# Optimization experiments

Hardware: AMD Instinct MI355X
Metric: run time of the kernel (lower is better)

## Reference

```python
import jax, jax.numpy as jnp
import numpy as np

IN_CH = 512
SCALES = (128.0, 256.0, 512.0)
ASPECT_RATIOS = (0.5, 1.0, 2.0)
NUM_ANCHORS = 9
PRE_NMS_TOPK = 10000
POST_NMS_TOPK = 2000
NMS_THRESH = 0.7


def conv2d(x, w, b, pad):
    y = jax.lax.conv_general_dilated(
        x, w, window_strides=(1, 1), padding=[(pad, pad), (pad, pad)],
        dimension_numbers=('NCHW', 'OIHW', 'NCHW'))
    return y + b[None, :, None, None]


def generate_anchors(image_hw, feat_hw, dtype=jnp.float32):
    img_h, img_w = image_hw
    gh, gw = feat_hw
    stride_h = img_h // gh
    stride_w = img_w // gw
    scale = jnp.asarray(SCALES, dtype)
    ar = jnp.asarray(ASPECT_RATIOS, dtype)
    h_ratio = jnp.sqrt(ar)
    w_ratio = 1.0 / h_ratio
    ws = (w_ratio[:, None] * scale[None, :]).reshape(-1)  # (9,) ratio-major
    hs = (h_ratio[:, None] * scale[None, :]).reshape(-1)
    base = jnp.round(jnp.stack([-ws, -hs, ws, hs], axis=1) / 2.0)  # (9,4)
    shift_x = jnp.arange(gw, dtype=dtype) * stride_w
    shift_y = jnp.arange(gh, dtype=dtype) * stride_h
    sy, sx = jnp.meshgrid(shift_y, shift_x, indexing='ij')
    sx = sx.reshape(-1)
    sy = sy.reshape(-1)
    shifts = jnp.stack([sx, sy, sx, sy], axis=1)  # (gh*gw, 4)
    anchors = (shifts[:, None, :] + base[None, :, :]).reshape(-1, 4)
    return anchors


def decode_boxes(deltas, anchors):
    # deltas: (N,4) [dx,dy,dw,dh]; anchors: (N,4) [x1,y1,x2,y2]
    w = anchors[:, 2] - anchors[:, 0]
    h = anchors[:, 3] - anchors[:, 1]
    cx = anchors[:, 0] + 0.5 * w
    cy = anchors[:, 1] + 0.5 * h
    dx, dy, dw, dh = deltas[:, 0], deltas[:, 1], deltas[:, 2], deltas[:, 3]
    pcx = w * dx + cx
    pcy = h * dy + cy
    pw = jnp.exp(dw) * w
    ph = jnp.exp(dh) * h
    return jnp.stack([pcx - 0.5 * pw, pcy - 0.5 * ph,
                      pcx + 0.5 * pw, pcy + 0.5 * ph], axis=1)


def clamp_boxes(b, image_hw):
    h, w = image_hw
    return jnp.stack([jnp.clip(b[:, 0], 0.0, w), jnp.clip(b[:, 1], 0.0, h),
                      jnp.clip(b[:, 2], 0.0, w), jnp.clip(b[:, 3], 0.0, h)], axis=1)


def pairwise_iou(boxes1, boxes2):
    area1 = (boxes1[:, 2] - boxes1[:, 0]) * (boxes1[:, 3] - boxes1[:, 1])
    area2 = (boxes2[:, 2] - boxes2[:, 0]) * (boxes2[:, 3] - boxes2[:, 1])
    xl = jnp.maximum(boxes1[:, None, 0], boxes2[None, :, 0])
    yt = jnp.maximum(boxes1[:, None, 1], boxes2[None, :, 1])
    xr = jnp.minimum(boxes1[:, None, 2], boxes2[None, :, 2])
    yb = jnp.minimum(boxes1[:, None, 3], boxes2[None, :, 3])
    inter = jnp.clip(xr - xl, 0.0) * jnp.clip(yb - yt, 0.0)
    return inter / (area1[:, None] + area2[None, :] - inter)


def nms_keep(boxes_sorted, thresh):
    # boxes already sorted by score descending; returns bool keep mask
    n = boxes_sorted.shape[0]
    iou = pairwise_iou(boxes_sorted, boxes_sorted)  # (n,n) ~ the memory-bound hot spot
    idx = jnp.arange(n)
    def body(i, keep):
        suppressed = jnp.any((iou[i] > thresh) & keep & (idx < i))
        return keep.at[i].set(jnp.logical_not(suppressed))
    return jax.lax.fori_loop(0, n, body, jnp.ones((n,), dtype=bool))


def filter_proposals(proposals, logits, image_hw):
    scores = jax.nn.sigmoid(logits.reshape(-1))
    top_scores, top_idx = jax.lax.top_k(scores, PRE_NMS_TOPK)  # sorted descending
    props = proposals[top_idx]
    props = clamp_boxes(props, image_hw)
    keep = nms_keep(jax.lax.stop_gradient(props), NMS_THRESH)
    masked = jnp.where(keep, jax.lax.stop_gradient(top_scores), -1.0)
    sel_scores, sel = jax.lax.top_k(masked, POST_NMS_TOPK)
    valid = sel_scores >= 0.0  # sigmoid scores are >0; padded slots are -1
    out_boxes = jnp.where(valid[:, None], props[sel], 0.0)
    out_scores = jnp.where(valid, top_scores[sel], 0.0)
    return out_boxes, out_scores


def setup_inputs() -> dict:
    key = jax.random.key(0)
    ks = jax.random.split(key, 6)
    image = jax.random.normal(ks[0], (1, 3, 800, 800), jnp.float32)
    feat = jax.random.normal(ks[1], (1, IN_CH, 50, 50), jnp.float32)
    # small init scales keep exp(dw) numerically tame (mimics real conv init)
    rpn_w = jax.random.normal(ks[2], (IN_CH, IN_CH, 3, 3), jnp.float32) * 0.02
    rpn_b = jnp.zeros((IN_CH,), jnp.float32)
    cls_w = jax.random.normal(ks[3], (NUM_ANCHORS, IN_CH, 1, 1), jnp.float32) * 0.01
    cls_b = jnp.zeros((NUM_ANCHORS,), jnp.float32)
    box_w = jax.random.normal(ks[4], (NUM_ANCHORS * 4, IN_CH, 1, 1), jnp.float32) * 0.01
    box_b = jnp.zeros((NUM_ANCHORS * 4,), jnp.float32)
    return {"image": image, "feat": feat, "rpn_w": rpn_w, "rpn_b": rpn_b,
            "cls_w": cls_w, "cls_b": cls_b, "box_w": box_w, "box_b": box_b}


def reference(image, feat, rpn_w, rpn_b, cls_w, cls_b, box_w, box_b):
    B, _, H, W = feat.shape  # B == 1 as in the original (single-image RPN)
    rpn_feat = jax.nn.relu(conv2d(feat, rpn_w, rpn_b, pad=1))
    cls = conv2d(rpn_feat, cls_w, cls_b, pad=0)        # (1, 9, H, W)
    box = conv2d(rpn_feat, box_w, box_b, pad=0)        # (1, 36, H, W)
    anchors = generate_anchors(image.shape[-2:], (H, W), feat.dtype)  # (H*W*9, 4)
    # cls: NCHW -> NHWC -> (N_anchors, 1), anchor order = (y, x, anchor)
    cls_flat = jnp.transpose(cls, (0, 2, 3, 1)).reshape(-1, 1)
    # box: (1,9,4,H,W) -> (1,H,W,9,4) -> (N_anchors, 4)
    deltas = jnp.transpose(box.reshape(B, NUM_ANCHORS, 4, H, W), (0, 3, 4, 1, 2)).reshape(-1, 4)
    proposals = decode_boxes(deltas, anchors)
    props, scores = filter_proposals(proposals, jax.lax.stop_gradient(cls_flat), image.shape[-2:])
    return props, scores, cls_flat
```

## Files before the change

kernel.cpp:

```cpp
#include <hip/hip_runtime.h>
#include <cstdint>
#include <cstddef>


typedef unsigned long long ull;
typedef double d4 __attribute__((ext_vector_type(4)));

#define NANCH 9
#define NPIX  2500
#define CIN   512
#define COUT  512
#define KTOT  4608
#define KSEG  2304
#define NBOX  22500
#define TOPK1 10000
#define TOPK2 2000
#define WORDS 157
#define NHEAD 45
#define HPAD  48

__global__ __launch_bounds__(128, 3) void conv_gemm(const float* __restrict__ feat,
                                                    const float* __restrict__ w,
                                                    double* __restrict__ part) {
  const int p0  = blockIdx.x * 32;
  const int co0 = blockIdx.y * 64;
  const int z   = blockIdx.z;
  const int kseg0 = z * KSEG;
  __shared__ float As[2][32][40];
  __shared__ float Bs[2][32][72];
  const int tid  = threadIdx.x;
  const int lane = tid & 63;
  const int wave = tid >> 6;
  const int quad = lane >> 4;
  const int l16  = lane & 15;
  const int wp = wave * 16;
  const int plB = tid & 31;
  const int kB0 = tid >> 5;
  const int pB = p0 + plB;
  const int py = pB / 50, px = pB - py * 50;
  const int coA = tid >> 1;
  const int kA2 = (tid & 1) * 16;

  int pmap[4];
  {
    double av_p = (quad == 0) ? (double)(l16 + 1) : (quad == 1 ? 1.0 : 0.0);
    double bv_p = (quad == 0) ? 1.0 : (quad == 1 ? (double)(1000 * (l16 + 1)) : 0.0);
    d4 dp = (d4){0.0, 0.0, 0.0, 0.0};
    dp = __builtin_amdgcn_mfma_f64_16x16x4f64(av_p, bv_p, dp, 0, 0, 0);
#pragma unroll
    for (int r = 0; r < 4; ++r) {
      int iv = (int)(dp[r] + 0.5);
      int mm = iv % 1000 - 1;
      int nn = iv / 1000 - 1;
      pmap[r] = (mm & 255) | (nn << 8);
    }
  }

  d4 acc[4];
#pragma unroll
  for (int i = 0; i < 4; ++i) acc[i] = (d4){0.0, 0.0, 0.0, 0.0};

  const float* wbase = w + (size_t)(co0 + coA) * KTOT + kseg0 + kA2;
  const int NCH = KSEG / 32;

  {
    float4 w0[4];
#pragma unroll
    for (int q = 0; q < 4; ++q) w0[q] = *(const float4*)(wbase + 4 * q);
    float f0[8];
#pragma unroll
    for (int jj = 0; jj < 8; ++jj) {
      int k = kseg0 + kB0 + 4 * jj;
      int ci = k / 9, r = k - ci * 9, ky = r / 3, kx = r - ky * 3;
      int yy = py + ky - 1, xx = px + kx - 1;
      float v = 0.0f;
      if (pB < NPIX && yy >= 0 && yy < 50 && xx >= 0 && xx < 50)
        v = feat[ci * NPIX + yy * 50 + xx];
      f0[jj] = v;
    }
#pragma unroll
    for (int q = 0; q < 4; ++q) {
      Bs[0][kA2 + 4 * q + 0][coA] = w0[q].x;
      Bs[0][kA2 + 4 * q + 1][coA] = w0[q].y;
      Bs[0][kA2 + 4 * q + 2][coA] = w0[q].z;
      Bs[0][kA2 + 4 * q + 3][coA] = w0[q].w;
    }
#pragma unroll
    for (int jj = 0; jj < 8; ++jj) As[0][kB0 + 4 * jj][plB] = f0[jj];
  }
  float4 wb1[4];
#pragma unroll
  for (int q = 0; q < 4; ++q) wb1[q] = *(const float4*)(wbase + 32 + 4 * q);
  float fb1[8];
#pragma unroll
  for (int jj = 0; jj < 8; ++jj) {
    int k = kseg0 + 32 + kB0 + 4 * jj;
    int ci = k / 9, r = k - ci * 9, ky = r / 3, kx = r - ky * 3;
    int yy = py + ky - 1, xx = px + kx - 1;
    float v = 0.0f;
    if (pB < NPIX && yy >= 0 && yy < 50 && xx >= 0 && xx < 50)
      v = feat[ci * NPIX + yy * 50 + xx];
    fb1[jj] = v;
  }
  __syncthreads();

  for (int c = 0; c < NCH; ++c) {
    const int buf = c & 1;
    if (c + 1 < NCH) {
#pragma unroll
      for (int q = 0; q < 4; ++q) {
        Bs[buf ^ 1][kA2 + 4 * q + 0][coA] = wb1[q].x;
        Bs[buf ^ 1][kA2 + 4 * q + 1][coA] = wb1[q].y;
        Bs[buf ^ 1][kA2 + 4 * q + 2][coA] = wb1[q].z;
        Bs[buf ^ 1][kA2 + 4 * q + 3][coA] = wb1[q].w;
      }
#pragma unroll
      for (int jj = 0; jj < 8; ++jj)
        As[buf ^ 1][kB0 + 4 * jj][plB] = fb1[jj];
    }
    if (c + 2 < NCH) {
#pragma unroll
      for (int q = 0; q < 4; ++q)
        wb1[q] = *(const float4*)(wbase + (c + 2) * 32 + 4 * q);
#pragma unroll
      for (int jj = 0; jj < 8; ++jj) {
        int k = kseg0 + (c + 2) * 32 + kB0 + 4 * jj;
        int ci = k / 9, r = k - ci * 9, ky = r / 3, kx = r - ky * 3;
        int yy = py + ky - 1, xx = px + kx - 1;
        float v = 0.0f;
        if (pB < NPIX && yy >= 0 && yy < 50 && xx >= 0 && xx < 50)
          v = feat[ci * NPIX + yy * 50 + xx];
        fb1[jj] = v;
      }
    }
#pragma unroll
    for (int kk = 0; kk < 32; kk += 4) {
      double av  = (double)As[buf][kk + quad][wp + l16];
      double bv0 = (double)Bs[buf][kk + quad][ 0 + l16];
      double bv1 = (double)Bs[buf][kk + quad][16 + l16];
      double bv2 = (double)Bs[buf][kk + quad][32 + l16];
      double bv3 = (double)Bs[buf][kk + quad][48 + l16];
      acc[0] = __builtin_amdgcn_mfma_f64_16x16x4f64(av, bv0, acc[0], 0, 0, 0);
      acc[1] = __builtin_amdgcn_mfma_f64_16x16x4f64(av, bv1, acc[1], 0, 0, 0);
      acc[2] = __builtin_amdgcn_mfma_f64_16x16x4f64(av, bv2, acc[2], 0, 0, 0);
      acc[3] = __builtin_amdgcn_mfma_f64_16x16x4f64(av, bv3, acc[3], 0, 0, 0);
    }
    __syncthreads();
  }
  double* basez = part + (size_t)z * COUT * NPIX;
#pragma unroll
  for (int cj = 0; cj < 4; ++cj) {
#pragma unroll
    for (int r = 0; r < 4; ++r) {
      int mm = pmap[r] & 255, nn = pmap[r] >> 8;
      int p  = p0 + wp + mm;
      int co = co0 + cj * 16 + nn;
      if (p < NPIX) basez[(size_t)co * NPIX + p] = acc[cj][r];
    }
  }
}

__global__ __launch_bounds__(256) void heads_mm(
    const double* __restrict__ part, const float* __restrict__ rpn_b,
    const float* __restrict__ cls_w, const float* __restrict__ box_w,
    double* __restrict__ headsc) {
  const int lane = threadIdx.x & 63;
  const int o = __builtin_amdgcn_readfirstlane(blockIdx.y * 4 + (threadIdx.x >> 6));
  if (o >= NHEAD) return;
  const int p = blockIdx.x * 64 + lane;
  const bool act = p < NPIX;
  const int pp = act ? p : 0;
  const float* wsel = (o < 9) ? (cls_w + (size_t)o * CIN)
                              : (box_w + (size_t)(o - 9) * CIN);
  const double* p0 = part + pp;
  const double* p1 = part + (size_t)COUT * NPIX + pp;
  double acc = 0.0;
#pragma unroll 4
  for (int co = 0; co < CIN; ++co) {
    double v = p0[(size_t)co * NPIX] + p1[(size_t)co * NPIX] + (double)rpn_b[co];
    v = v > 0.0 ? v : 0.0;
    acc += (double)wsel[co] * v;
  }
  if (act) headsc[(size_t)p * HPAD + o] = acc;
}

__global__ __launch_bounds__(256) void decode_kernel(
    const double* __restrict__ headsc, const float* __restrict__ cls_b,
    const float* __restrict__ box_b, double* __restrict__ logits,
    double* __restrict__ boxesAll, float* __restrict__ out_cls) {
  int idx = blockIdx.x * blockDim.x + threadIdx.x;
  if (idx >= NBOX) return;
  int p = idx / 9, a = idx - p * 9;
  int y = p / 50, x = p - y * 50;
  double sx = 16.0 * (double)x, sy = 16.0 * (double)y;
  const double scs[3] = {128.0, 256.0, 512.0};
  const double ars[3] = {0.5, 1.0, 2.0};
  double ar = ars[a / 3], sc = scs[a - (a / 3) * 3];
  double hr = sqrt(ar), wr = 1.0 / hr;
  double wv = wr * sc, hv = hr * sc;
  double bx0 = rint(-wv * 0.5), by0 = rint(-hv * 0.5);
  double bx1 = rint(wv * 0.5), by1 = rint(hv * 0.5);
  double a0 = sx + bx0, a1 = sy + by0, a2 = sx + bx1, a3 = sy + by1;
  double wA = a2 - a0, hA = a3 - a1;
  double cx = a0 + 0.5 * wA, cy = a1 + 0.5 * hA;
  const double* hp = headsc + (size_t)p * HPAD;
  double dx = hp[9 + a * 4 + 0] + (double)box_b[a * 4 + 0];
  double dy = hp[9 + a * 4 + 1] + (double)box_b[a * 4 + 1];
  double dw = hp[9 + a * 4 + 2] + (double)box_b[a * 4 + 2];
  double dh = hp[9 + a * 4 + 3] + (double)box_b[a * 4 + 3];
  double pcx = wA * dx + cx, pcy = hA * dy + cy;
  double pw = exp(dw) * wA, ph = exp(dh) * hA;
  double b0 = pcx - 0.5 * pw, b1 = pcy - 0.5 * ph;
  double b2 = pcx + 0.5 * pw, b3 = pcy + 0.5 * ph;
  b0 = fmin(fmax(b0, 0.0), 800.0);
  b1 = fmin(fmax(b1, 0.0), 800.0);
  b2 = fmin(fmax(b2, 0.0), 800.0);
  b3 = fmin(fmax(b3, 0.0), 800.0);
  boxesAll[(size_t)idx * 4 + 0] = b0;
  boxesAll[(size_t)idx * 4 + 1] = b1;
  boxesAll[(size_t)idx * 4 + 2] = b2;
  boxesAll[(size_t)idx * 4 + 3] = b3;
  double L = hp[a] + (double)cls_b[a];
  logits[idx] = L;
  out_cls[idx] = (float)L;
}

__global__ __launch_bounds__(256) void rank_count(const double* __restrict__ logits,
                                                  int* __restrict__ ranks) {
  __shared__ double Ls[2048];
  int i = blockIdx.x * 256 + threadIdx.x;
  int j0 = blockIdx.y * 2048;
  int jn = NBOX - j0;
  if (jn > 2048) jn = 2048;
  for (int t = threadIdx.x; t < jn; t += 256) Ls[t] = logits[j0 + t];
  __syncthreads();
  if (i >= NBOX) return;
  double Li = logits[i];
  int cnt = 0;
  for (int t = 0; t < jn; ++t) {
    double Lj = Ls[t];
    int j = j0 + t;
    cnt += (Lj > Li || (Lj == Li && j < i)) ? 1 : 0;
  }
  atomicAdd(&ranks[i], cnt);
}

__global__ __launch_bounds__(256) void scatter_topk(const double* __restrict__ logits,
                                                    const double* __restrict__ boxesAll,
                                                    const int* __restrict__ ranks,
                                                    double* __restrict__ sLog,
                                                    double* __restrict__ sBox) {
  int i = blockIdx.x * 256 + threadIdx.x;
  if (i >= NBOX) return;
  int r = ranks[i];
  if (r < TOPK1) {
    sLog[r] = logits[i];
    sBox[(size_t)r * 4 + 0] = boxesAll[(size_t)i * 4 + 0];
    sBox[(size_t)r * 4 + 1] = boxesAll[(size_t)i * 4 + 1];
    sBox[(size_t)r * 4 + 2] = boxesAll[(size_t)i * 4 + 2];
    sBox[(size_t)r * 4 + 3] = boxesAll[(size_t)i * 4 + 3];
  }
}

__global__ __launch_bounds__(256) void iou_mask(const double* __restrict__ sb,
                                                ull* __restrict__ mask) {
  const int it = blockIdx.x;
  const int wt = blockIdx.y;
  if (wt * 4 + 3 < it) return;
  __shared__ double ib[64][4];
  __shared__ double jb[256][4];
  const int tid = threadIdx.x;
  {
    int ii = it * 64 + (tid >> 2);
    int d = tid & 3;
    ib[tid >> 2][d] = (ii < TOPK1) ? sb[(size_t)ii * 4 + d] : 0.0;
  }
  for (int t = tid; t < 1024; t += 256) {
    int jj = wt * 256 + (t >> 2);
    jb[t >> 2][t & 3] = (jj < TOPK1) ? sb[(size_t)jj * 4 + (t & 3)] : 0.0;
  }
  __syncthreads();
  const int il = tid & 63, wl = tid >> 6;
  const int i = it * 64 + il;
  const int word = wt * 4 + wl;
  if (i >= TOPK1 || word >= WORDS || word < (i >> 6)) return;
  const double x0 = ib[il][0], y0 = ib[il][1], x1 = ib[il][2], y1 = ib[il][3];
  const double areai = (x1 - x0) * (y1 - y0);
  ull bits = 0;
  const int jbase = word * 64;
  for (int b = 0; b < 64; ++b) {
    int j = jbase + b;
    if (j <= i || j >= TOPK1) continue;
    int jl = wl * 64 + b;
    double u0 = jb[jl][0], u1 = jb[jl][1], u2 = jb[jl][2], u3 = jb[jl][3];
    double xl = fmax(x0, u0), yt = fmax(y0, u1);
    double xr = fmin(x1, u2), yb = fmin(y1, u3);
    double iw = xr - xl, ih = yb - yt;
    iw = iw > 0.0 ? iw : 0.0;
    ih = ih > 0.0 ? ih : 0.0;
    double inter = iw * ih;
    double aj = (u2 - u0) * (u3 - u1);
    double un = areai + aj - inter;
    if (inter > 0.7 * un) bits |= 1ull << b;
  }
  mask[(size_t)i * WORDS + word] = bits;
}

#define NTILE 8
#define TRS   10
#define KCAP  2112

__global__ __launch_bounds__(256) void nms_scan(const ull* __restrict__ mask,
                                                ull* __restrict__ keepwords) {
  __shared__ ull tileRows[512 * TRS];
  __shared__ int klist[KCAP];
  __shared__ ull remvPart[32][NTILE + 1];
  __shared__ unsigned int remv32[NTILE * 2];
  __shared__ int newk[64];
  __shared__ int kcLds, nkLds, doneLds;
  const int tid = threadIdx.x;
  const int lane = tid & 63;
  const int wave = tid >> 6;
  if (tid == 0) { kcLds = 0; nkLds = 0; doneLds = 0; }
  __syncthreads();

  for (int T = 0; T < (WORDS + NTILE - 1) / NTILE; ++T) {
    const int G0 = T * NTILE;
    const int TW = (WORDS - G0 < NTILE) ? (WORDS - G0) : NTILE;
    const int kc0 = kcLds;
#pragma unroll
    for (int pass = 0; pass < 8; ++pass) {
      int lr = pass * 64 + (tid >> 2);
      int w  = (tid & 3) * 2;
      int gr = G0 * 64 + lr;
      ull v0 = 0, v1 = 0;
      if (gr < TOPK1) {
        const ull* row = mask + (size_t)gr * WORDS + G0;
        if (w < TW)     v0 = row[w];
        if (w + 1 < TW) v1 = row[w + 1];
      }
      tileRows[lr * TRS + w]     = v0;
      tileRows[lr * TRS + w + 1] = v1;
    }
    {
      int w = tid & 7, stripe = tid >> 3;
      ull acc = 0;
      if (w < TW) {
        int t = stripe;
        for (; t + 224 < kc0; t += 256) {
          ull a0 = mask[(size_t)klist[t      ] * WORDS + G0 + w];
          ull a1 = mask[(size_t)klist[t +  32] * WORDS + G0 + w];
          ull a2 = mask[(size_t)klist[t +  64] * WORDS + G0 + w];
          ull a3 = mask[(size_t)klist[t +  96] * WORDS + G0 + w];
          ull a4 = mask[(size_t)klist[t + 128] * WORDS + G0 + w];
          ull a5 = mask[(size_t)klist[t + 160] * WORDS + G0 + w];
          ull a6 = mask[(size_t)klist[t + 192] * WORDS + G0 + w];
          ull a7 = mask[(size_t)klist[t + 224] * WORDS + G0 + w];
          acc |= ((a0 | a1) | (a2 | a3)) | ((a4 | a5) | (a6 | a7));
        }
        for (; t < kc0; t += 32) acc |= mask[(size_t)klist[t] * WORDS + G0 + w];
      }
      remvPart[stripe][w] = acc;
    }
    __syncthreads();
    if (tid < NTILE) {
      ull r = 0;
#pragma unroll
      for (int s = 0; s < 32; ++s) r |= remvPart[s][tid];
      remv32[tid * 2]     = (unsigned int)r;
      remv32[tid * 2 + 1] = (unsigned int)(r >> 32);
    }
    __syncthreads();
    for (int gi = 0; gi < TW; ++gi) {
      const int g = G0 + gi;
      if (wave == 0) {
        ull cur = ((ull)remv32[gi * 2 + 1] << 32) | remv32[gi * 2];
        unsigned int clo = __builtin_amdgcn_readfirstlane((unsigned int)cur);
        unsigned int chi = __builtin_amdgcn_readfirstlane((unsigned int)(cur >> 32));
        cur = ((ull)chi << 32) | clo;
        ull mrow = tileRows[(gi * 64 + lane) * TRS + gi];
        const unsigned int ml = (unsigned int)mrow;
        const unsigned int mh = (unsigned int)(mrow >> 32);
        const ull validm = (g == WORDS - 1) ? 0xFFFFull : ~0ull;
        ull rem = (~cur) & validm;
        while (rem) {
          int b = __ffsll((long long)rem) - 1;
          b = __builtin_amdgcn_readfirstlane(b);
          ull m = ((ull)(unsigned int)__builtin_amdgcn_readlane((int)mh, b) << 32) |
                  (unsigned int)__builtin_amdgcn_readlane((int)ml, b);
          cur |= m;
          ull above = (b == 63) ? 0ull : (~0ull << (b + 1));
          rem = (~cur) & rem & above;
        }
        ull kb = (~cur) & validm;
        if (lane == 0) keepwords[g] = kb;
        int kc = kcLds;
        if ((kb >> lane) & 1ull) {
          int ofs = __popcll(lane ? (kb & ((1ull << lane) - 1ull)) : 0ull);
          klist[kc + ofs] = g * 64 + lane;
          newk[ofs] = gi * 64 + lane;
        }
        if (lane == 0) {
          int nk = __popcll(kb);
          nkLds = nk;
          kcLds = kc + nk;
          doneLds = (kc + nk >= TOPK2) ? 1 : 0;
        }
      }
      __syncthreads();
      if (doneLds) break;
      if (gi + 1 < TW) {
        int w = tid & 7, k0 = tid >> 3;
        int nk = nkLds;
        if (w > gi && w < TW) {
          ull acc = 0;
          for (int kk = k0; kk < nk; kk += 32) acc |= tileRows[newk[kk] * TRS + w];
          if (acc) {
            atomicOr(&remv32[w * 2], (unsigned int)acc);
            atomicOr(&remv32[w * 2 + 1], (unsigned int)(acc >> 32));
          }
        }
      }
      __syncthreads();
    }
    if (doneLds) break;
  }
}

__global__ __launch_bounds__(256) void finalize_kernel(const ull* __restrict__ keepwords,
                                                       const double* __restrict__ sBox,
                                                       const double* __restrict__ sLog,
                                                       float* __restrict__ out) {
  __shared__ int pref[WORDS];
  int t = threadIdx.x;
  if (t == 0) {
    int s = 0;
    for (int w = 0; w < WORDS; ++w) {
      pref[w] = s;
      s += __popcll(keepwords[w]);
    }
  }
  __syncthreads();
  if (t < WORDS) {
    ull kb = keepwords[t];
    int base = pref[t];
    while (kb) {
      int b = __ffsll((long long)kb) - 1;
      kb &= kb - 1;
      if (base < TOPK2) {
        int i = t * 64 + b;
        out[base * 4 + 0] = (float)sBox[(size_t)i * 4 + 0];
        out[base * 4 + 1] = (float)sBox[(size_t)i * 4 + 1];
        out[base * 4 + 2] = (float)sBox[(size_t)i * 4 + 2];
        out[base * 4 + 3] = (float)sBox[(size_t)i * 4 + 3];
        double L = sLog[i];
        out[TOPK2 * 4 + base] = (float)(1.0 / (1.0 + exp(-L)));
      }
      ++base;
    }
  }
}

extern "C" void kernel_launch(void* const* d_in, const int* in_sizes, int n_in,
                              void* d_out, int out_size, void* d_ws, size_t ws_size,
                              hipStream_t stream) {
  const float* feat  = (const float*)d_in[1];
  const float* rpn_w = (const float*)d_in[2];
  const float* rpn_b = (const float*)d_in[3];
  const float* cls_w = (const float*)d_in[4];
  const float* cls_b = (const float*)d_in[5];
  const float* box_w = (const float*)d_in[6];
  const float* box_b = (const float*)d_in[7];
  float* out = (float*)d_out;

  char* ws = (char*)d_ws;
  double* part     = (double*)(ws);
  double* logits   = (double*)(ws + 20480000);
  double* boxesAll = (double*)(ws + 20660000);
  int*    ranks    = (int*)   (ws + 21380000);
  double* sBox     = (double*)(ws + 21470000);
  double* sLog     = (double*)(ws + 21790000);
  ull*    mask     = (ull*)   (ws + 21870000);
  ull*    keepw    = (ull*)   (ws + 34430000);
  double* headsc   = (double*)(ws + 21870000);

  hipMemsetAsync(d_out, 0, (TOPK2 * 4 + TOPK2) * sizeof(float), stream);
  hipMemsetAsync(ranks, 0, NBOX * sizeof(int), stream);
  hipMemsetAsync(keepw, 0, WORDS * sizeof(ull), stream);

  conv_gemm<<<dim3(80, 8, 2), 128, 0, stream>>>(feat, rpn_w, part);
  heads_mm<<<dim3(40, 12), 256, 0, stream>>>(part, rpn_b, cls_w, box_w, headsc);
  decode_kernel<<<88, 256, 0, stream>>>(headsc, cls_b, box_b, logits, boxesAll,
                                        out + TOPK2 * 5);
  rank_count<<<dim3(88, 11), 256, 0, stream>>>(logits, ranks);
  scatter_topk<<<88, 256, 0, stream>>>(logits, boxesAll, ranks, sLog, sBox);
  iou_mask<<<dim3(WORDS, 40), 256, 0, stream>>>(sBox, mask);
  nms_scan<<<1, 256, 0, stream>>>(mask, keepw);
  finalize_kernel<<<1, 256, 0, stream>>>(keepw, sBox, sLog, out);
}
```

Before: 873.1 us.

## Pre-transpose conv weights to tap-major layout and simplify im2col indexing

Adds a kernel that reorders the 3x3 conv weights from [co][ci][tap] to [tap][ci][co]. The GEMM then walks K in tap-major order, so each 32-wide K chunk shares one (ky,kx) tap. That replaces the per-element div/mod im2col math and per-element bounds checks with one computation per chunk, and lets weight loads be coalesced along co. The cost is an extra launch plus a 9 MB transpose of the weights on every call, stored in workspace that aliases the headsc/mask region.

```diff
diff --git a/kernel.cpp b/kernel.cpp
--- a/kernel.cpp
+++ b/kernel.cpp
@@ -19,8 +19,28 @@
 #define NHEAD 45
 #define HPAD  48
 
+__global__ __launch_bounds__(256) void wtrans(const float* __restrict__ w,
+                                              float* __restrict__ wT) {
+  __shared__ float t[36][65];
+  const int ci0 = blockIdx.x * 4;
+  const int co0 = blockIdx.y * 64;
+  const int tid = threadIdx.x;
+  const int co_l = tid >> 2, cq = tid & 3;
+  const float* src = w + (size_t)(co0 + co_l) * KTOT + (ci0 + cq) * 9;
+#pragma unroll
+  for (int r = 0; r < 9; ++r) t[r * 4 + cq][co_l] = src[r];
+  __syncthreads();
+  const int co_w = tid & 63, rw0 = tid >> 6;
+#pragma unroll
+  for (int m = 0; m < 9; ++m) {
+    int rw = rw0 + 4 * m;
+    int tap = rw >> 2, cqq = rw & 3;
+    wT[((size_t)tap * 512 + ci0 + cqq) * 512 + co0 + co_w] = t[rw][co_w];
+  }
+}
+
 __global__ __launch_bounds__(128, 3) void conv_gemm(const float* __restrict__ feat,
-                                                    const float* __restrict__ w,
+                                                    const float* __restrict__ wT,
                                                     double* __restrict__ part) {
   const int p0  = blockIdx.x * 32;
   const int co0 = blockIdx.y * 64;
@@ -34,12 +54,10 @@
   const int quad = lane >> 4;
   const int l16  = lane & 15;
   const int wp = wave * 16;
-  const int plB = tid & 31;
-  const int kB0 = tid >> 5;
-  const int pB = p0 + plB;
+  const int plA = tid & 31, kAr = tid >> 5;
+  const int pB = p0 + plA;
   const int py = pB / 50, px = pB - py * 50;
-  const int coA = tid >> 1;
-  const int kA2 = (tid & 1) * 16;
+  const int coB = tid & 63, kBr = tid >> 6;
 
   int pmap[4];
   {
@@ -60,78 +78,52 @@
 #pragma unroll
   for (int i = 0; i < 4; ++i) acc[i] = (d4){0.0, 0.0, 0.0, 0.0};
 
-  const float* wbase = w + (size_t)(co0 + coA) * KTOT + kseg0 + kA2;
   const int NCH = KSEG / 32;
 
-  {
-    float4 w0[4];
-#pragma unroll
-    for (int q = 0; q < 4; ++q) w0[q] = *(const float4*)(wbase + 4 * q);
-    float f0[8];
+  float fa[8], fb[16];
+
+  auto loadA = [&](int cc) {
+    int kk0 = kseg0 + cc * 32;
+    int tap = kk0 >> 9;
+    int ci0 = kk0 & 511;
+    int ky = (tap * 11) >> 5;
+    int kx = tap - 3 * ky;
+    int yy = py + ky - 1, xx = px + kx - 1;
+    bool valid = (pB < NPIX) && (yy >= 0) && (yy < 50) && (xx >= 0) && (xx < 50);
+    int off = valid ? ((ci0 + kAr) * NPIX + yy * 50 + xx) : 0;
 #pragma unroll
     for (int jj = 0; jj < 8; ++jj) {
-      int k = kseg0 + kB0 + 4 * jj;
-      int ci = k / 9, r = k - ci * 9, ky = r / 3, kx = r - ky * 3;
-      int yy = py + ky - 1, xx = px + kx - 1;
-      float v = 0.0f;
-      if (pB < NPIX && yy >= 0 && yy < 50 && xx >= 0 && xx < 50)
-        v = feat[ci * NPIX + yy * 50 + xx];
-      f0[jj] = v;
-    }
-#pragma unroll
-    for (int q = 0; q < 4; ++q) {
-      Bs[0][kA2 + 4 * q + 0][coA] = w0[q].x;
-      Bs[0][kA2 + 4 * q + 1][coA] = w0[q].y;
-      Bs[0][kA2 + 4 * q + 2][coA] = w0[q].z;
-      Bs[0][kA2 + 4 * q + 3][coA] = w0[q].w;
-    }
-#pragma unroll
-    for (int jj = 0; jj < 8; ++jj) As[0][kB0 + 4 * jj][plB] = f0[jj];
-  }
-  float4 wb1[4];
-#pragma unroll
-  for (int q = 0; q < 4; ++q) wb1[q] = *(const float4*)(wbase + 32 + 4 * q);
-  float fb1[8];
-#pragma unroll
-  for (int jj = 0; jj < 8; ++jj) {
-    int k = kseg0 + 32 + kB0 + 4 * jj;
-    int ci = k / 9, r = k - ci * 9, ky = r / 3, kx = r - ky * 3;
-    int yy = py + ky - 1, xx = px + kx - 1;
-    float v = 0.0f;
-    if (pB < NPIX && yy >= 0 && yy < 50 && xx >= 0 && xx < 50)
-      v = feat[ci * NPIX + yy * 50 + xx];
-    fb1[jj] = v;
-  }
+      float v = feat[off + jj * 4 * NPIX];
+      fa[jj] = valid ? v : 0.0f;
+    }
+  };
+  auto loadB = [&](int cc) {
+    const float* src = wT + (size_t)(kseg0 + cc * 32 + kBr) * 512 + co0 + coB;
+#pragma unroll
+    for (int s = 0; s < 16; ++s) fb[s] = src[s * 2 * 512];
+  };
+
+  loadA(0);
+  loadB(0);
+#pragma unroll
+  for (int jj = 0; jj < 8; ++jj) As[0][kAr + 4 * jj][plA] = fa[jj];
+#pragma unroll
+  for (int s = 0; s < 16; ++s) Bs[0][kBr + 2 * s][coB] = fb[s];
+  loadA(1);
+  loadB(1);
   __syncthreads();
 
   for (int c = 0; c < NCH; ++c) {
     const int buf = c & 1;
     if (c + 1 < NCH) {
 #pragma unroll
-      for (int q = 0; q < 4; ++q) {
-        Bs[buf ^ 1][kA2 + 4 * q + 0][coA] = wb1[q].x;
-        Bs[buf ^ 1][kA2 + 4 * q + 1][coA] = wb1[q].y;
-        Bs[buf ^ 1][kA2 + 4 * q + 2][coA] = wb1[q].z;
-        Bs[buf ^ 1][kA2 + 4 * q + 3][coA] = wb1[q].w;
-      }
-#pragma unroll
-      for (int jj = 0; jj < 8; ++jj)
-        As[buf ^ 1][kB0 + 4 * jj][plB] = fb1[jj];
+      for (int jj = 0; jj < 8; ++jj) As[buf ^ 1][kAr + 4 * jj][plA] = fa[jj];
+#pragma unroll
+      for (int s = 0; s < 16; ++s) Bs[buf ^ 1][kBr + 2 * s][coB] = fb[s];
     }
     if (c + 2 < NCH) {
-#pragma unroll
-      for (int q = 0; q < 4; ++q)
-        wb1[q] = *(const float4*)(wbase + (c + 2) * 32 + 4 * q);
-#pragma unroll
-      for (int jj = 0; jj < 8; ++jj) {
-        int k = kseg0 + (c + 2) * 32 + kB0 + 4 * jj;
-        int ci = k / 9, r = k - ci * 9, ky = r / 3, kx = r - ky * 3;
-        int yy = py + ky - 1, xx = px + kx - 1;
-        float v = 0.0f;
-        if (pB < NPIX && yy >= 0 && yy < 50 && xx >= 0 && xx < 50)
-          v = feat[ci * NPIX + yy * 50 + xx];
-        fb1[jj] = v;
-      }
+      loadA(c + 2);
+      loadB(c + 2);
     }
 #pragma unroll
     for (int kk = 0; kk < 32; kk += 4) {
@@ -482,13 +474,15 @@
   double* sLog     = (double*)(ws + 21790000);
   ull*    mask     = (ull*)   (ws + 21870000);
   ull*    keepw    = (ull*)   (ws + 34430000);
+  float*  wT       = (float*) (ws + 21870000);
   double* headsc   = (double*)(ws + 21870000);
 
   hipMemsetAsync(d_out, 0, (TOPK2 * 4 + TOPK2) * sizeof(float), stream);
   hipMemsetAsync(ranks, 0, NBOX * sizeof(int), stream);
   hipMemsetAsync(keepw, 0, WORDS * sizeof(ull), stream);
 
-  conv_gemm<<<dim3(80, 8, 2), 128, 0, stream>>>(feat, rpn_w, part);
+  wtrans<<<dim3(128, 8), 256, 0, stream>>>(rpn_w, wT);
+  conv_gemm<<<dim3(80, 8, 2), 128, 0, stream>>>(feat, wT, part);
   heads_mm<<<dim3(40, 12), 256, 0, stream>>>(part, rpn_b, cls_w, box_w, headsc);
   decode_kernel<<<88, 256, 0, stream>>>(headsc, cls_b, box_b, logits, boxesAll,
                                         out + TOPK2 * 5);
```

Measured after the change: 832.7 us. 1.05x faster.
